# Performance work log

Hardware: AMD Instinct MI355X
Metric: run time of the kernel (lower is better)

Reference implementation:

```python
import jax, jax.numpy as jnp
import numpy as np

HEADS = 4
DIM_HEAD = 64


def _rope(x, inv_freq):
    """Interleaved rotary embedding over axis -2 (time). x: (N, h, T, d)."""
    T = x.shape[-2]
    t = jnp.arange(T, dtype=x.dtype)
    f = t[:, None] * inv_freq[None, :].astype(x.dtype)   # (T, d/2)
    f = jnp.repeat(f, 2, axis=-1)                        # (T, d), interleaved pairs
    cos, sin = jnp.cos(f), jnp.sin(f)
    x1, x2 = x[..., 0::2], x[..., 1::2]
    rot = jnp.stack([-x2, x1], axis=-1).reshape(x.shape)  # rotate_half, interleaved
    return x * cos + rot * sin


def setup_inputs() -> dict:
    key = jax.random.key(0)
    k1, k2, k3, k4 = jax.random.split(key, 4)
    B, T, H, W, D = 2, 64, 32, 32, 256
    inner = HEADS * DIM_HEAD
    x = jax.random.normal(k1, (B, T, H, W, D), dtype=jnp.float32)
    w_qkv = jax.random.normal(k2, (D, 3 * inner), dtype=jnp.float32) * 0.02
    w_out = jax.random.normal(k3, (inner, D), dtype=jnp.float32) * 0.02
    b_out = jax.random.normal(k4, (D,), dtype=jnp.float32) * 0.02
    # rotary-embedding-torch default: 1 / theta^(arange(0, d, 2)/d)
    inv_freq = (1.0 / (10000.0 ** (np.arange(0, DIM_HEAD, 2) / DIM_HEAD))).astype(np.float32)
    return {"x": x, "w_qkv": w_qkv, "w_out": w_out, "b_out": b_out,
            "inv_freq": jnp.asarray(inv_freq)}


def reference(x, w_qkv, w_out, b_out, inv_freq):
    B, T, H, W, D = x.shape
    h, d = HEADS, DIM_HEAD
    qkv = x @ w_qkv                                   # (B,T,H,W,3*inner)
    q, k, v = jnp.split(qkv, 3, axis=-1)

    def to_heads(t_):
        # B T H W (h d) -> (B H W) h T d
        t_ = t_.reshape(B, T, H, W, h, d)
        return t_.transpose(0, 2, 3, 4, 1, 5).reshape(B * H * W, h, T, d)

    q, k, v = map(to_heads, (q, k, v))
    q = _rope(q, inv_freq)
    k = _rope(k, inv_freq)

    scale = 1.0 / np.sqrt(d).astype(np.float32)
    scores = jnp.einsum('nhtd,nhsd->nhts', q, k) * scale  # (BHW, h, T, T)
    causal = jnp.tril(jnp.ones((T, T), dtype=bool))
    scores = jnp.where(causal, scores, jnp.finfo(scores.dtype).min)
    attn = jax.nn.softmax(scores, axis=-1)
    o = jnp.einsum('nhts,nhsd->nhtd', attn, v)            # (BHW, h, T, d)

    # (B H W) h T d -> B T H W (h d)
    o = o.reshape(B, H, W, h, T, d).transpose(0, 4, 1, 2, 3, 5).reshape(B, T, H, W, h * d)
    return o @ w_out + b_out
```

## Files before the change

### kernel.cpp

```cpp
#include <hip/hip_runtime.h>
#include <hip/hip_bf16.h>

typedef __bf16 bf16_t;
typedef bf16_t bf16x4 __attribute__((ext_vector_type(4)));
typedef bf16_t bf16x8 __attribute__((ext_vector_type(8)));
typedef float f32x4 __attribute__((ext_vector_type(4)));

#define MFMA16(a, b, c) __builtin_amdgcn_mfma_f32_16x16x32_bf16((a), (b), (c), 0, 0, 0)

__device__ __forceinline__ int sxi(int row, int e) { return row * 256 + (e ^ ((row & 7) << 3)); }
__device__ __forceinline__ int ski(int row, int e) { return row * 64 + (e ^ ((row & 7) << 3)); }

__global__ void transpose_to_bf16(const float* __restrict__ in, bf16_t* __restrict__ outp,
                                  int K, int N) {
  __shared__ float tile[32][33];
  const int k0 = blockIdx.x * 32;
  const int n0 = blockIdx.y * 32;
  const int tx = threadIdx.x;
  const int ty = threadIdx.y;
#pragma unroll
  for (int i = 0; i < 32; i += 8)
    tile[ty + i][tx] = in[(size_t)(k0 + ty + i) * N + (n0 + tx)];
  __syncthreads();
#pragma unroll
  for (int i = 0; i < 32; i += 8)
    outp[(size_t)(n0 + ty + i) * K + (k0 + tx)] = (bf16_t)tile[tx][ty + i];
}

__global__ void rope_table(const float* __restrict__ invf, float2* __restrict__ cs) {
  const int idx = blockIdx.x * 256 + threadIdx.x;
  const int t = idx >> 5;
  const int i = idx & 31;
  const float f = (float)t * invf[i];
  cs[idx] = make_float2(cosf(f), sinf(f));
}

__global__ __launch_bounds__(256, 2) void taa_fused(
    const float* __restrict__ x, const bf16_t* __restrict__ wqkvT,
    const bf16_t* __restrict__ woutT, const float* __restrict__ bout,
    const float2* __restrict__ ropecs, float* __restrict__ out) {
  __shared__ __attribute__((aligned(16))) bf16_t sX[64 * 256];
  __shared__ __attribute__((aligned(16))) bf16_t sK[4][64 * 64];

  const int tid = threadIdx.x;
  const int w = tid >> 6;
  const int l = tid & 63;
  const int l16 = l & 15;
  const int g = l >> 4;

  const int wg = blockIdx.x;
  const int b = wg >> 10;
  const int sp = wg & 1023;

  const size_t TS = 1024 * 256;
  const float* xp = x + (size_t)((b * 64) * 1024 + sp) * 256;
  float* op = out + (size_t)((b * 64) * 1024 + sp) * 256;

#pragma unroll
  for (int it = 0; it < 16; ++it) {
    const int idx = tid + it * 256;
    const int t = idx >> 6;
    const int c = (idx & 63) * 4;
    const float4 v = *(const float4*)(xp + (size_t)t * TS + c);
    bf16x4 o4;
    o4[0] = (bf16_t)v.x; o4[1] = (bf16_t)v.y; o4[2] = (bf16_t)v.z; o4[3] = (bf16_t)v.w;
    *(bf16x4*)&sX[sxi(t, c)] = o4;
  }
  __syncthreads();

  f32x4 qacc[4][4] = {};
  f32x4 vacc[4][4] = {};
  {
#pragma unroll
    for (int k0 = 0; k0 < 256; k0 += 32) {
      const int ko = k0 + 8 * g;
      bf16x8 af[4], bf[4];
#pragma unroll
      for (int m = 0; m < 4; ++m) af[m] = *(const bf16x8*)&sX[sxi(16 * m + l16, ko)];
#pragma unroll
      for (int n = 0; n < 4; ++n)
        bf[n] = *(const bf16x8*)&wqkvT[(size_t)(w * 64 + 16 * n + l16) * 256 + ko];
#pragma unroll
      for (int m = 0; m < 4; ++m)
#pragma unroll
        for (int n = 0; n < 4; ++n) qacc[m][n] = MFMA16(af[m], bf[n], qacc[m][n]);
    }
    const float qs = 0.125f * 1.44269504088896f;
#pragma unroll
    for (int m = 0; m < 4; ++m)
#pragma unroll
      for (int n = 0; n < 4; ++n)
#pragma unroll
        for (int r = 0; r < 4; ++r) {
          const int t = 16 * m + 4 * g + r, dd = 16 * n + l16;
          const float v = qacc[m][n][r];
          const float p = __shfl_xor(v, 1);
          const float2 cs = ropecs[t * 32 + (dd >> 1)];
          const float o = (dd & 1) ? (v * cs.x + p * cs.y) : (v * cs.x - p * cs.y);
          qacc[m][n][r] = o * qs;
        }
    f32x4 kacc[4][4] = {};
#pragma unroll
    for (int k0 = 0; k0 < 256; k0 += 32) {
      const int ko = k0 + 8 * g;
      bf16x8 af[4], bf[4];
#pragma unroll
      for (int m = 0; m < 4; ++m) af[m] = *(const bf16x8*)&sX[sxi(16 * m + l16, ko)];
#pragma unroll
      for (int n = 0; n < 4; ++n)
        bf[n] = *(const bf16x8*)&wqkvT[(size_t)(256 + w * 64 + 16 * n + l16) * 256 + ko];
#pragma unroll
      for (int m = 0; m < 4; ++m)
#pragma unroll
        for (int n = 0; n < 4; ++n) kacc[m][n] = MFMA16(af[m], bf[n], kacc[m][n]);
    }
#pragma unroll
    for (int m = 0; m < 4; ++m)
#pragma unroll
      for (int n = 0; n < 4; ++n)
#pragma unroll
        for (int r = 0; r < 4; ++r) {
          const int s = 16 * m + 4 * g + r, dd = 16 * n + l16;
          const float v = kacc[m][n][r];
          const float p = __shfl_xor(v, 1);
          const float2 cs = ropecs[s * 32 + (dd >> 1)];
          const float o = (dd & 1) ? (v * cs.x + p * cs.y) : (v * cs.x - p * cs.y);
          sK[w][ski(s, dd)] = (bf16_t)o;
        }
#pragma unroll
    for (int k0 = 0; k0 < 256; k0 += 32) {
      const int ko = k0 + 8 * g;
      bf16x8 af[4], bf[4];
#pragma unroll
      for (int m = 0; m < 4; ++m) af[m] = *(const bf16x8*)&sX[sxi(16 * m + l16, ko)];
#pragma unroll
      for (int n = 0; n < 4; ++n)
        bf[n] = *(const bf16x8*)&wqkvT[(size_t)(512 + w * 64 + 16 * n + l16) * 256 + ko];
#pragma unroll
      for (int m = 0; m < 4; ++m)
#pragma unroll
        for (int n = 0; n < 4; ++n) vacc[m][n] = MFMA16(af[m], bf[n], vacc[m][n]);
    }
  }
  __syncthreads();

  bf16_t* slice = &sX[w * 4096];
#pragma unroll
  for (int m = 0; m < 4; ++m)
#pragma unroll
    for (int n = 0; n < 4; ++n)
#pragma unroll
      for (int r = 0; r < 4; ++r) {
        const int t = 16 * m + 4 * g + r, dd = 16 * n + l16;
        slice[ski(t, dd)] = (bf16_t)qacc[m][n][r];
      }

  f32x4 sc[4][4] = {};
#pragma unroll
  for (int ks = 0; ks < 2; ++ks) {
    const int ko = ks * 32 + 8 * g;
    bf16x8 af[4], bf[4];
#pragma unroll
    for (int m = 0; m < 4; ++m) af[m] = *(const bf16x8*)&sK[w][ski(16 * m + l16, ko)];
#pragma unroll
    for (int n = 0; n < 4; ++n) bf[n] = *(const bf16x8*)&slice[ski(16 * n + l16, ko)];
#pragma unroll
    for (int m = 0; m < 4; ++m)
#pragma unroll
      for (int n = 0; n < 4; ++n) sc[m][n] = MFMA16(af[m], bf[n], sc[m][n]);
  }

#pragma unroll
  for (int n = 0; n < 4; ++n) {
    const int t = 16 * n + l16;
    float vals[16];
    float mx = -3.0e38f;
#pragma unroll
    for (int m = 0; m < 4; ++m)
#pragma unroll
      for (int r = 0; r < 4; ++r) {
        const int s = 16 * m + 4 * g + r;
        const float v = (s <= t) ? sc[m][n][r] : -3.0e38f;
        vals[4 * m + r] = v;
        mx = fmaxf(mx, v);
      }
    mx = fmaxf(mx, __shfl_xor(mx, 16));
    mx = fmaxf(mx, __shfl_xor(mx, 32));
    float sum = 0.f;
#pragma unroll
    for (int i = 0; i < 16; ++i) {
      vals[i] = exp2f(vals[i] - mx);
      sum += vals[i];
    }
    sum += __shfl_xor(sum, 16);
    sum += __shfl_xor(sum, 32);
    const float inv = 1.0f / sum;
#pragma unroll
    for (int m = 0; m < 4; ++m) {
      bf16x4 p4;
#pragma unroll
      for (int r = 0; r < 4; ++r) p4[r] = (bf16_t)(vals[4 * m + r] * inv);
      *(bf16x4*)&slice[ski(t, 16 * m + 4 * g)] = p4;
    }
  }

  f32x4 oacc[4][4] = {};
#pragma unroll
  for (int ks = 0; ks < 2; ++ks) {
    const int ko = ks * 32 + 8 * g;
    bf16x8 af[4];
#pragma unroll
    for (int m = 0; m < 4; ++m) af[m] = *(const bf16x8*)&slice[ski(16 * m + l16, ko)];
    bf16x8 bfv[4];
    const int srcA = (2 * (g & 1)) * 16 + l16;
#pragma unroll
    for (int n = 0; n < 4; ++n) {
      bf16x8 f;
#pragma unroll
      for (int h = 0; h < 2; ++h) {
        const int src = srcA + h * 16;
#pragma unroll
        for (int r = 0; r < 4; ++r) {
          const float v0 = __shfl(vacc[2 * ks][n][r], src);
          const float v1 = __shfl(vacc[2 * ks + 1][n][r], src);
          f[4 * h + r] = (bf16_t)((g & 2) ? v1 : v0);
        }
      }
      bfv[n] = f;
    }
#pragma unroll
    for (int m = 0; m < 4; ++m)
#pragma unroll
      for (int n = 0; n < 4; ++n) oacc[m][n] = MFMA16(af[m], bfv[n], oacc[m][n]);
  }
  __syncthreads();

#pragma unroll
  for (int m = 0; m < 4; ++m)
#pragma unroll
    for (int n = 0; n < 4; ++n)
#pragma unroll
      for (int r = 0; r < 4; ++r) {
        const int t = 16 * m + 4 * g + r, col = w * 64 + 16 * n + l16;
        sX[sxi(t, col)] = (bf16_t)oacc[m][n][r];
      }
  __syncthreads();

  f32x4 acc[4][4] = {};
#pragma unroll
  for (int k0 = 0; k0 < 256; k0 += 32) {
    const int ko = k0 + 8 * g;
    bf16x8 af[4], bf[4];
#pragma unroll
    for (int m = 0; m < 4; ++m) af[m] = *(const bf16x8*)&sX[sxi(16 * m + l16, ko)];
#pragma unroll
    for (int n = 0; n < 4; ++n)
      bf[n] = *(const bf16x8*)&woutT[(size_t)(w * 64 + 16 * n + l16) * 256 + ko];
#pragma unroll
    for (int m = 0; m < 4; ++m)
#pragma unroll
      for (int n = 0; n < 4; ++n) acc[m][n] = MFMA16(af[m], bf[n], acc[m][n]);
  }
  float bb[4];
#pragma unroll
  for (int n = 0; n < 4; ++n) bb[n] = bout[w * 64 + 16 * n + l16];
#pragma unroll
  for (int m = 0; m < 4; ++m)
#pragma unroll
    for (int n = 0; n < 4; ++n)
#pragma unroll
      for (int r = 0; r < 4; ++r) {
        const int t = 16 * m + 4 * g + r, col = w * 64 + 16 * n + l16;
        op[(size_t)t * TS + col] = acc[m][n][r] + bb[n];
      }
}

extern "C" void kernel_launch(void* const* d_in, const int* in_sizes, int n_in,
                              void* d_out, int out_size, void* d_ws, size_t ws_size,
                              hipStream_t stream) {
  const float* x = (const float*)d_in[0];
  const float* wqkv = (const float*)d_in[1];
  const float* wout = (const float*)d_in[2];
  const float* bout = (const float*)d_in[3];
  const float* invf = (const float*)d_in[4];
  float* out = (float*)d_out;

  char* ws = (char*)d_ws;
  bf16_t* wqkvT = (bf16_t*)ws;
  bf16_t* woutT = (bf16_t*)(ws + 393216);
  float2* ropecs = (float2*)(ws + 393216 + 131072);

  transpose_to_bf16<<<dim3(8, 24), dim3(32, 8), 0, stream>>>(wqkv, wqkvT, 256, 768);
  transpose_to_bf16<<<dim3(8, 8), dim3(32, 8), 0, stream>>>(wout, woutT, 256, 256);
  rope_table<<<8, 256, 0, stream>>>(invf, ropecs);

  taa_fused<<<2048, 256, 0, stream>>>(x, wqkvT, woutT, bout, ropecs, out);
}
```

Baseline: 246.5 us.

## Cut LDS and register footprint to fit three workgroups per CU

Drops the per-wave sK shared buffer and keeps Q in registers as packed bf16, computed transposed so RoPE pairs sit in the same lane without shuffles. The V projection moves to after the softmax, with x reloaded from global memory, so the V accumulators no longer live alongside Q/K. Launch bounds rise to 3 blocks per CU. In exchange it adds more cross-lane shuffles to rebuild the Q and V operands, and a second global read of x for the V GEMM.

```diff
diff --git a/kernel.cpp b/kernel.cpp
--- a/kernel.cpp
+++ b/kernel.cpp
@@ -5,11 +5,18 @@
 typedef bf16_t bf16x4 __attribute__((ext_vector_type(4)));
 typedef bf16_t bf16x8 __attribute__((ext_vector_type(8)));
 typedef float f32x4 __attribute__((ext_vector_type(4)));
+typedef unsigned int u32;
 
 #define MFMA16(a, b, c) __builtin_amdgcn_mfma_f32_16x16x32_bf16((a), (b), (c), 0, 0, 0)
 
 __device__ __forceinline__ int sxi(int row, int e) { return row * 256 + (e ^ ((row & 7) << 3)); }
 __device__ __forceinline__ int ski(int row, int e) { return row * 64 + (e ^ ((row & 7) << 3)); }
+
+__device__ __forceinline__ u32 pk2(float a, float b) {
+  union { bf16_t h[2]; u32 u; } x;
+  x.h[0] = (bf16_t)a; x.h[1] = (bf16_t)b;
+  return x.u;
+}
 
 __global__ void transpose_to_bf16(const float* __restrict__ in, bf16_t* __restrict__ outp,
                                   int K, int N) {
@@ -35,12 +42,11 @@
   cs[idx] = make_float2(cosf(f), sinf(f));
 }
 
-__global__ __launch_bounds__(256, 2) void taa_fused(
+__global__ __launch_bounds__(256, 3) void taa_fused(
     const float* __restrict__ x, const bf16_t* __restrict__ wqkvT,
     const bf16_t* __restrict__ woutT, const float* __restrict__ bout,
     const float2* __restrict__ ropecs, float* __restrict__ out) {
   __shared__ __attribute__((aligned(16))) bf16_t sX[64 * 256];
-  __shared__ __attribute__((aligned(16))) bf16_t sK[4][64 * 64];
 
   const int tid = threadIdx.x;
   const int w = tid >> 6;
@@ -48,9 +54,9 @@
   const int l16 = l & 15;
   const int g = l >> 4;
 
-  const int wg = blockIdx.x;
-  const int b = wg >> 10;
-  const int sp = wg & 1023;
+  const int site = blockIdx.x;
+  const int b = site >> 10;
+  const int sp = site & 1023;
 
   const size_t TS = 1024 * 256;
   const float* xp = x + (size_t)((b * 64) * 1024 + sp) * 256;
@@ -68,22 +74,22 @@
   }
   __syncthreads();
 
-  f32x4 qacc[4][4] = {};
-  f32x4 vacc[4][4] = {};
+  u32 qtb[4][4][2];
   {
+    f32x4 qt[4][4] = {};
 #pragma unroll
     for (int k0 = 0; k0 < 256; k0 += 32) {
       const int ko = k0 + 8 * g;
-      bf16x8 af[4], bf[4];
-#pragma unroll
-      for (int m = 0; m < 4; ++m) af[m] = *(const bf16x8*)&sX[sxi(16 * m + l16, ko)];
-#pragma unroll
-      for (int n = 0; n < 4; ++n)
-        bf[n] = *(const bf16x8*)&wqkvT[(size_t)(w * 64 + 16 * n + l16) * 256 + ko];
+      bf16x8 aw[4], bx[4];
 #pragma unroll
       for (int m = 0; m < 4; ++m)
-#pragma unroll
-        for (int n = 0; n < 4; ++n) qacc[m][n] = MFMA16(af[m], bf[n], qacc[m][n]);
+        aw[m] = *(const bf16x8*)&wqkvT[(size_t)(w * 64 + 16 * m + l16) * 256 + ko];
+#pragma unroll
+      for (int n = 0; n < 4; ++n) bx[n] = *(const bf16x8*)&sX[sxi(16 * n + l16, ko)];
+#pragma unroll
+      for (int m = 0; m < 4; ++m)
+#pragma unroll
+        for (int n = 0; n < 4; ++n) qt[m][n] = MFMA16(aw[m], bx[n], qt[m][n]);
     }
     const float qs = 0.125f * 1.44269504088896f;
 #pragma unroll
@@ -91,28 +97,28 @@
 #pragma unroll
       for (int n = 0; n < 4; ++n)
 #pragma unroll
-        for (int r = 0; r < 4; ++r) {
-          const int t = 16 * m + 4 * g + r, dd = 16 * n + l16;
-          const float v = qacc[m][n][r];
-          const float p = __shfl_xor(v, 1);
-          const float2 cs = ropecs[t * 32 + (dd >> 1)];
-          const float o = (dd & 1) ? (v * cs.x + p * cs.y) : (v * cs.x - p * cs.y);
-          qacc[m][n][r] = o * qs;
+        for (int c = 0; c < 2; ++c) {
+          const float v0 = qt[m][n][2 * c], v1 = qt[m][n][2 * c + 1];
+          const float2 cs = ropecs[(16 * n + l16) * 32 + 8 * m + 2 * g + c];
+          qtb[m][n][c] = pk2((v0 * cs.x - v1 * cs.y) * qs, (v1 * cs.x + v0 * cs.y) * qs);
         }
-    f32x4 kacc[4][4] = {};
+  }
+
+  f32x4 ka[4][4] = {};
+  {
 #pragma unroll
     for (int k0 = 0; k0 < 256; k0 += 32) {
       const int ko = k0 + 8 * g;
-      bf16x8 af[4], bf[4];
-#pragma unroll
-      for (int m = 0; m < 4; ++m) af[m] = *(const bf16x8*)&sX[sxi(16 * m + l16, ko)];
-#pragma unroll
-      for (int n = 0; n < 4; ++n)
-        bf[n] = *(const bf16x8*)&wqkvT[(size_t)(256 + w * 64 + 16 * n + l16) * 256 + ko];
+      bf16x8 ax[4], bw[4];
+#pragma unroll
+      for (int m = 0; m < 4; ++m) ax[m] = *(const bf16x8*)&sX[sxi(16 * m + l16, ko)];
+#pragma unroll
+      for (int n = 0; n < 4; ++n)
+        bw[n] = *(const bf16x8*)&wqkvT[(size_t)(256 + w * 64 + 16 * n + l16) * 256 + ko];
 #pragma unroll
       for (int m = 0; m < 4; ++m)
 #pragma unroll
-        for (int n = 0; n < 4; ++n) kacc[m][n] = MFMA16(af[m], bf[n], kacc[m][n]);
+        for (int n = 0; n < 4; ++n) ka[m][n] = MFMA16(ax[m], bw[n], ka[m][n]);
     }
 #pragma unroll
     for (int m = 0; m < 4; ++m)
@@ -120,27 +126,13 @@
       for (int n = 0; n < 4; ++n)
 #pragma unroll
         for (int r = 0; r < 4; ++r) {
-          const int s = 16 * m + 4 * g + r, dd = 16 * n + l16;
-          const float v = kacc[m][n][r];
+          const float v = ka[m][n][r];
           const float p = __shfl_xor(v, 1);
-          const float2 cs = ropecs[s * 32 + (dd >> 1)];
-          const float o = (dd & 1) ? (v * cs.x + p * cs.y) : (v * cs.x - p * cs.y);
-          sK[w][ski(s, dd)] = (bf16_t)o;
+          const int s = 16 * m + 4 * g + r;
+          const int dd = 16 * n + l16;
+          const float2 cs = ropecs[s * 32 + 8 * n + (l16 >> 1)];
+          ka[m][n][r] = (dd & 1) ? (v * cs.x + p * cs.y) : (v * cs.x - p * cs.y);
         }
-#pragma unroll
-    for (int k0 = 0; k0 < 256; k0 += 32) {
-      const int ko = k0 + 8 * g;
-      bf16x8 af[4], bf[4];
-#pragma unroll
-      for (int m = 0; m < 4; ++m) af[m] = *(const bf16x8*)&sX[sxi(16 * m + l16, ko)];
-#pragma unroll
-      for (int n = 0; n < 4; ++n)
-        bf[n] = *(const bf16x8*)&wqkvT[(size_t)(512 + w * 64 + 16 * n + l16) * 256 + ko];
-#pragma unroll
-      for (int m = 0; m < 4; ++m)
-#pragma unroll
-        for (int n = 0; n < 4; ++n) vacc[m][n] = MFMA16(af[m], bf[n], vacc[m][n]);
-    }
   }
   __syncthreads();
 
@@ -150,24 +142,33 @@
 #pragma unroll
     for (int n = 0; n < 4; ++n)
 #pragma unroll
-      for (int r = 0; r < 4; ++r) {
-        const int t = 16 * m + 4 * g + r, dd = 16 * n + l16;
-        slice[ski(t, dd)] = (bf16_t)qacc[m][n][r];
-      }
+      for (int r = 0; r < 4; ++r)
+        slice[ski(16 * m + 4 * g + r, 16 * n + l16)] = (bf16_t)ka[m][n][r];
 
   f32x4 sc[4][4] = {};
 #pragma unroll
   for (int ks = 0; ks < 2; ++ks) {
     const int ko = ks * 32 + 8 * g;
-    bf16x8 af[4], bf[4];
-#pragma unroll
-    for (int m = 0; m < 4; ++m) af[m] = *(const bf16x8*)&sK[w][ski(16 * m + l16, ko)];
-#pragma unroll
-    for (int n = 0; n < 4; ++n) bf[n] = *(const bf16x8*)&slice[ski(16 * n + l16, ko)];
-#pragma unroll
-    for (int m = 0; m < 4; ++m)
-#pragma unroll
-      for (int n = 0; n < 4; ++n) sc[m][n] = MFMA16(af[m], bf[n], sc[m][n]);
+    bf16x8 ak[4];
+#pragma unroll
+    for (int m = 0; m < 4; ++m) ak[m] = *(const bf16x8*)&slice[ski(16 * m + l16, ko)];
+    bf16x8 bq[4];
+#pragma unroll
+    for (int n = 0; n < 4; ++n) {
+      union { u32 u[4]; bf16x8 v; } uu;
+#pragma unroll
+      for (int k2 = 0; k2 < 4; ++k2) {
+        const int src = ((((2 * g + (k2 >> 1)) & 3) << 4) | l16);
+        const u32 a0 = (u32)__shfl((int)qtb[2 * ks][n][k2 & 1], src);
+        const u32 a1 = (u32)__shfl((int)qtb[2 * ks + 1][n][k2 & 1], src);
+        uu.u[k2] = (g & 2) ? a1 : a0;
+      }
+      bq[n] = uu.v;
+    }
+#pragma unroll
+    for (int m = 0; m < 4; ++m)
+#pragma unroll
+      for (int n = 0; n < 4; ++n) sc[m][n] = MFMA16(ak[m], bq[n], sc[m][n]);
   }
 
 #pragma unroll
@@ -204,34 +205,63 @@
     }
   }
 
+  u32 vb[4][4][2];
+  {
+    f32x4 va[4][4] = {};
+#pragma unroll
+    for (int k0 = 0; k0 < 256; k0 += 32) {
+      const int ko = k0 + 8 * g;
+      bf16x8 ax[4], bw[4];
+#pragma unroll
+      for (int m = 0; m < 4; ++m) {
+        const float* xr = xp + (size_t)(16 * m + l16) * TS + ko;
+        const float4 u = *(const float4*)xr;
+        const float4 v = *(const float4*)(xr + 4);
+        union { u32 q[4]; bf16x8 h; } cv;
+        cv.q[0] = pk2(u.x, u.y); cv.q[1] = pk2(u.z, u.w);
+        cv.q[2] = pk2(v.x, v.y); cv.q[3] = pk2(v.z, v.w);
+        ax[m] = cv.h;
+      }
+#pragma unroll
+      for (int n = 0; n < 4; ++n)
+        bw[n] = *(const bf16x8*)&wqkvT[(size_t)(512 + w * 64 + 16 * n + l16) * 256 + ko];
+#pragma unroll
+      for (int m = 0; m < 4; ++m)
+#pragma unroll
+        for (int n = 0; n < 4; ++n) va[m][n] = MFMA16(ax[m], bw[n], va[m][n]);
+    }
+#pragma unroll
+    for (int m = 0; m < 4; ++m)
+#pragma unroll
+      for (int n = 0; n < 4; ++n)
+#pragma unroll
+        for (int c = 0; c < 2; ++c) vb[m][n][c] = pk2(va[m][n][2 * c], va[m][n][2 * c + 1]);
+  }
+
   f32x4 oacc[4][4] = {};
 #pragma unroll
   for (int ks = 0; ks < 2; ++ks) {
     const int ko = ks * 32 + 8 * g;
-    bf16x8 af[4];
-#pragma unroll
-    for (int m = 0; m < 4; ++m) af[m] = *(const bf16x8*)&slice[ski(16 * m + l16, ko)];
-    bf16x8 bfv[4];
-    const int srcA = (2 * (g & 1)) * 16 + l16;
+    bf16x8 ap[4];
+#pragma unroll
+    for (int m = 0; m < 4; ++m) ap[m] = *(const bf16x8*)&slice[ski(16 * m + l16, ko)];
+    bf16x8 bv[4];
 #pragma unroll
     for (int n = 0; n < 4; ++n) {
-      bf16x8 f;
-#pragma unroll
-      for (int h = 0; h < 2; ++h) {
-        const int src = srcA + h * 16;
-#pragma unroll
-        for (int r = 0; r < 4; ++r) {
-          const float v0 = __shfl(vacc[2 * ks][n][r], src);
-          const float v1 = __shfl(vacc[2 * ks + 1][n][r], src);
-          f[4 * h + r] = (bf16_t)((g & 2) ? v1 : v0);
-        }
-      }
-      bfv[n] = f;
-    }
-#pragma unroll
-    for (int m = 0; m < 4; ++m)
-#pragma unroll
-      for (int n = 0; n < 4; ++n) oacc[m][n] = MFMA16(af[m], bfv[n], oacc[m][n]);
+      union { u32 u[4]; bf16x8 v; } uu;
+#pragma unroll
+      for (int k2 = 0; k2 < 4; ++k2) {
+        const int src = ((((2 * g + (k2 >> 1)) & 3) << 4) | l16);
+        const u32 a0 = (u32)__shfl((int)vb[2 * ks][n][k2 & 1], src);
+        const u32 a1 = (u32)__shfl((int)vb[2 * ks + 1][n][k2 & 1], src);
+        uu.u[k2] = (g & 2) ? a1 : a0;
+      }
+      bv[n] = uu.v;
+    }
+#pragma unroll
+    for (int m = 0; m < 4; ++m)
+#pragma unroll
+      for (int n = 0; n < 4; ++n) oacc[m][n] = MFMA16(ap[m], bv[n], oacc[m][n]);
   }
   __syncthreads();
 
@@ -240,10 +270,8 @@
 #pragma unroll
     for (int n = 0; n < 4; ++n)
 #pragma unroll
-      for (int r = 0; r < 4; ++r) {
-        const int t = 16 * m + 4 * g + r, col = w * 64 + 16 * n + l16;
-        sX[sxi(t, col)] = (bf16_t)oacc[m][n][r];
-      }
+      for (int r = 0; r < 4; ++r)
+        sX[sxi(16 * m + 4 * g + r, w * 64 + 16 * n + l16)] = (bf16_t)oacc[m][n][r];
   __syncthreads();
 
   f32x4 acc[4][4] = {};
@@ -270,7 +298,8 @@
     for (int n = 0; n < 4; ++n)
 #pragma unroll
       for (int r = 0; r < 4; ++r) {
-        const int t = 16 * m + 4 * g + r, col = w * 64 + 16 * n + l16;
+        const int t = 16 * m + 4 * g + r;
+        const int col = w * 64 + 16 * n + l16;
         op[(size_t)t * TS + col] = acc[m][n][r] + bb[n];
       }
 }
```

Result: slower. 509.6 us (+106.8%).
